# Kernel tuning notes

Measured on AMD Instinct MI355X. Metric: run time of the kernel, lower is better.

Reference implementation:

```python
import jax, jax.numpy as jnp
import numpy as np

DX, DZ, DT = 10.0, 10.0, 1.0e-3
NX, NZ = 512, 512
NSTEPS, NREC = 512, 128
DT2 = DT * DT
INV_DXDZ = 1.0 / (DX * DZ)


def setup_inputs() -> dict:
    key = jax.random.key(0)
    k1, k2, k3, k4 = jax.random.split(key, 4)
    # velocity in [1500, 2500] m/s -> CFL stable with dt=1e-3, dx=dz=10
    velocity_model = 1500.0 + 1000.0 * jax.random.uniform(k1, (NX, NZ), dtype=jnp.float32)
    source = jax.random.normal(k2, (NSTEPS,), dtype=jnp.float32)
    rec_x = jax.random.randint(k3, (NREC,), 0, NX)
    rec_z = jax.random.randint(k4, (NREC,), 0, NZ)
    return {
        "velocity_model": velocity_model,
        "source": source,
        "src_x": 256,
        "src_z": 8,
        "rec_x": rec_x,
        "rec_z": rec_z,
    }


def _laplacian(p):
    # 3x3 cross stencil with zero padding, scaled by 1/(dx*dz) -- identical to
    # F.conv2d(p, [[0,1,0],[1,-4,1],[0,1,0]]/(dx*dz), padding=1)
    pp = jnp.pad(p, 1)
    return (pp[:-2, 1:-1] + pp[2:, 1:-1] + pp[1:-1, :-2] + pp[1:-1, 2:] - 4.0 * p) * INV_DXDZ


def reference(velocity_model, source, src_x, src_z, rec_x, rec_z):
    v2_dt2 = velocity_model * velocity_model * DT2  # [nx, nz]

    def step(carry, s_t):
        p, p_old = carry
        p_new = 2.0 * p - p_old + v2_dt2 * _laplacian(p)
        p_new = p_new.at[src_x, src_z].add(s_t * DT2)
        return (p_new, p), p_new[rec_x, rec_z]  # gather all receivers at once

    p0 = jnp.zeros((NX, NZ), dtype=velocity_model.dtype)
    _, recs = jax.lax.scan(step, (p0, p0), source)  # recs: [n_steps, n_rec]
    return recs.T  # seismogram: [n_rec, n_steps]
```

## Files before the change

### kernel.cpp

```cpp
#include <hip/hip_runtime.h>


#define NXd 512
#define NZd 512
#define NSTEPSd 512
#define NRECd 128
#define DT2f 1.0e-6f
#define INVf 1.0e-2f
#define TBk 16
#define TIk 32
#define EXTk 64
#define NTILEk 16

__device__ __forceinline__ float dpp_shr1(float x) {
    int v = __builtin_amdgcn_update_dpp(0, __builtin_bit_cast(int, x),
                                        0x138, 0xF, 0xF, false);
    return __builtin_bit_cast(float, v);
}
__device__ __forceinline__ float dpp_shl1(float x) {
    int v = __builtin_amdgcn_update_dpp(0, __builtin_bit_cast(int, x),
                                        0x130, 0xF, 0xF, false);
    return __builtin_bit_cast(float, v);
}

__global__ __launch_bounds__(1024) void fdtd_tblock(
    const float* __restrict__ vel,
    const float* __restrict__ source,
    const int* __restrict__ src_x, const int* __restrict__ src_z,
    const int* __restrict__ rec_x, const int* __restrict__ rec_z,
    const float2* __restrict__ Pin, float2* __restrict__ Pout,
    float* __restrict__ out, int t0)
{
    __shared__ float sb[2][EXTk * EXTk];

    const int tid = threadIdx.x;
    const int w   = tid >> 6;
    const int ez  = tid & 63;
    const int gx0 = blockIdx.y * TIk, gz0 = blockIdx.x * TIk;
    const int ox = gx0 - TBk, oz = gz0 - TBk;
    const int gz = oz + ez;
    const bool zin = (gz >= 0 && gz < NZd);
    const int sx = *src_x, sz = *src_z;

    bool rOwn = false; int rIdx = 0;
    if (tid < NRECd) {
        int rx = rec_x[tid], rz = rec_z[tid];
        rOwn = (rx >= gx0 && rx < gx0 + TIk && rz >= gz0 && rz < gz0 + TIk);
        rIdx = (rx - ox) * EXTk + (rz - oz);
    }

    {
        int dxm = max(0, max(ox - sx, sx - (ox + EXTk - 1)));
        int dzm = max(0, max(oz - sz, sz - (oz + EXTk - 1)));
        if (dxm + dzm > t0 + TBk + 1) {
            if (rOwn) {
                #pragma unroll
                for (int s = 0; s < TBk; ++s)
                    out[tid * NSTEPSd + t0 + s] = 0.0f;
            }
            return;
        }
    }

    float rCur[4], rOld[4], rV2i[4];
    #pragma unroll
    for (int i = 0; i < 4; ++i) {
        const int ex = 4 * w + i;
        const int gx = ox + ex;
        float c = 0.0f, o = 0.0f, v2 = 0.0f;
        if (zin && gx >= 0 && gx < NXd) {
            const int g = gx * NZd + gz;
            float2 co = Pin[g];
            c = co.x; o = co.y;
            const float v = vel[g];
            v2 = v * v * (DT2f * INVf);
        }
        rCur[i] = c; rOld[i] = o; rV2i[i] = v2;
        sb[0][ex * EXTk + ez] = c;
    }
    const int rowUp = (w == 0)  ? 0        : 4 * w - 1;
    const int rowDn = (w == 15) ? EXTk - 1 : 4 * w + 4;

    const int exs = sx - ox, ezs = sz - oz;
    const bool srcHere = (exs >= 0 && exs < EXTk && ezs >= 0 && ezs < EXTk) &&
                         (tid == (((exs >> 2) << 6) | ezs));
    float sv[TBk];
    if (srcHere) {
        #pragma unroll
        for (int s = 0; s < TBk; ++s) sv[s] = source[t0 + s] * DT2f;
    }

    __syncthreads();

    float rv[TBk];
    #pragma unroll
    for (int s = 0; s < TBk; ++s) {
        const float* cur = sb[s & 1];
        float* nxt = sb[(s & 1) ^ 1];
        const float up0 = cur[rowUp * EXTk + ez];
        const float dn3 = cur[rowDn * EXTk + ez];
        float nv[4];
        #pragma unroll
        for (int i = 0; i < 4; ++i) {
            const float up = (i == 0) ? up0 : rCur[i - 1];
            const float dn = (i == 3) ? dn3 : rCur[i + 1];
            const float lf = dpp_shr1(rCur[i]);
            const float rt = dpp_shl1(rCur[i]);
            const float sum = (up + dn) + (lf + rt);
            const float t4 = __builtin_fmaf(-4.0f, rCur[i], sum);
            const float pm = __builtin_fmaf(2.0f, rCur[i], -rOld[i]);
            nv[i] = __builtin_fmaf(rV2i[i], t4, pm);
        }
        #pragma unroll
        for (int i = 0; i < 4; ++i) {
            rOld[i] = rCur[i];
            rCur[i] = nv[i];
            nxt[(4 * w + i) * EXTk + ez] = nv[i];
        }
        if (srcHere) {
            #pragma unroll
            for (int i = 0; i < 4; ++i) {
                if (i == (exs & 3)) {
                    rCur[i] += sv[s];
                    nxt[exs * EXTk + ezs] = rCur[i];
                }
            }
        }
        __syncthreads();
        if (rOwn) rv[s] = nxt[rIdx];
    }

    if (rOwn) {
        #pragma unroll
        for (int s = 0; s < TBk; ++s)
            out[tid * NSTEPSd + t0 + s] = rv[s];
    }

    if (w >= 4 && w < 12 && ez >= TBk && ez < EXTk - TBk) {
        #pragma unroll
        for (int i = 0; i < 4; ++i) {
            const int g = (ox + 4 * w + i) * NZd + gz;
            Pout[g] = make_float2(rCur[i], rOld[i]);
        }
    }
}

extern "C" void kernel_launch(void* const* d_in, const int* in_sizes, int n_in,
                              void* d_out, int out_size, void* d_ws, size_t ws_size,
                              hipStream_t stream) {
    const float* vel    = (const float*)d_in[0];
    const float* source = (const float*)d_in[1];
    const int*   src_x  = (const int*)d_in[2];
    const int*   src_z  = (const int*)d_in[3];
    const int*   rec_x  = (const int*)d_in[4];
    const int*   rec_z  = (const int*)d_in[5];
    float* out = (float*)d_out;

    const size_t F = (size_t)NXd * NZd;
    float2* PA = (float2*)d_ws;
    float2* PB = PA + F;

    hipMemsetAsync(d_ws, 0, 2 * F * sizeof(float2), stream);

    dim3 grid(NTILEk, NTILEk), block(1024);
    for (int k = 0; k < NSTEPSd / TBk; ++k) {
        const float2* Pin = (k & 1) ? PB : PA;
        float2* Pout      = (k & 1) ? PA : PB;
        fdtd_tblock<<<grid, block, 0, stream>>>(vel, source, src_x, src_z,
                                                rec_x, rec_z, Pin, Pout,
                                                out, k * TBk);
    }
}
```

Before: 365.0 us.

## Advance two time steps per barrier using redundant halo-row computation in registers

Each thread now reads two halo rows above and below from shared memory and also computes the neighbouring rows, so it can take two time steps per shared-memory exchange and cut the number of barriers and LDS round trips in half. Receivers are routed through shared-memory tables to the thread that owns the point, so readings come from registers instead of from LDS after each step. The cost is extra redundant arithmetic, more registers, extra global loads for the halo rows, and an atomic-based routing setup.

```diff
diff --git a/kernel.cpp b/kernel.cpp
--- a/kernel.cpp
+++ b/kernel.cpp
@@ -23,6 +23,20 @@
     return __builtin_bit_cast(float, v);
 }
 
+__device__ __forceinline__ float upd(float c, float o, float v2,
+                                     float up, float dn) {
+    float lf = dpp_shr1(c);
+    float rt = dpp_shl1(c);
+    float sum = (up + dn) + (lf + rt);
+    float t4 = __builtin_fmaf(-4.0f, c, sum);
+    float pm = __builtin_fmaf(2.0f, c, -o);
+    return __builtin_fmaf(v2, t4, pm);
+}
+
+__device__ __forceinline__ float sel4(int r, float a, float b, float c, float d) {
+    return (r == 0) ? a : (r == 1) ? b : (r == 2) ? c : d;
+}
+
 __global__ __launch_bounds__(1024) void fdtd_tblock(
     const float* __restrict__ vel,
     const float* __restrict__ source,
@@ -32,6 +46,7 @@
     float* __restrict__ out, int t0)
 {
     __shared__ float sb[2][EXTk * EXTk];
+    __shared__ int route0[1024], route1[1024], route2[1024];
 
     const int tid = threadIdx.x;
     const int w   = tid >> 6;
@@ -42,32 +57,27 @@
     const bool zin = (gz >= 0 && gz < NZd);
     const int sx = *src_x, sz = *src_z;
 
-    bool rOwn = false; int rIdx = 0;
-    if (tid < NRECd) {
-        int rx = rec_x[tid], rz = rec_z[tid];
-        rOwn = (rx >= gx0 && rx < gx0 + TIk && rz >= gz0 && rz < gz0 + TIk);
-        rIdx = (rx - ox) * EXTk + (rz - oz);
-    }
-
     {
         int dxm = max(0, max(ox - sx, sx - (ox + EXTk - 1)));
         int dzm = max(0, max(oz - sz, sz - (oz + EXTk - 1)));
         if (dxm + dzm > t0 + TBk + 1) {
-            if (rOwn) {
-                #pragma unroll
-                for (int s = 0; s < TBk; ++s)
-                    out[tid * NSTEPSd + t0 + s] = 0.0f;
+            if (tid < NRECd) {
+                int rx = rec_x[tid], rz = rec_z[tid];
+                if (rx >= gx0 && rx < gx0 + TIk && rz >= gz0 && rz < gz0 + TIk) {
+                    #pragma unroll
+                    for (int s = 0; s < TBk; ++s)
+                        out[tid * NSTEPSd + t0 + s] = 0.0f;
+                }
             }
             return;
         }
     }
 
-    float rCur[4], rOld[4], rV2i[4];
+    float rCur[4], rOld[4], rV2[4];
     #pragma unroll
     for (int i = 0; i < 4; ++i) {
-        const int ex = 4 * w + i;
-        const int gx = ox + ex;
-        float c = 0.0f, o = 0.0f, v2 = 0.0f;
+        const int gx = ox + 4 * w + i;
+        float c = 0.f, o = 0.f, v2 = 0.f;
         if (zin && gx >= 0 && gx < NXd) {
             const int g = gx * NZd + gz;
             float2 co = Pin[g];
@@ -75,65 +85,109 @@
             const float v = vel[g];
             v2 = v * v * (DT2f * INVf);
         }
-        rCur[i] = c; rOld[i] = o; rV2i[i] = v2;
-        sb[0][ex * EXTk + ez] = c;
-    }
-    const int rowUp = (w == 0)  ? 0        : 4 * w - 1;
-    const int rowDn = (w == 15) ? EXTk - 1 : 4 * w + 4;
+        rCur[i] = c; rOld[i] = o; rV2[i] = v2;
+        sb[0][(4 * w + i) * EXTk + ez] = c;
+    }
+    float rOldX0 = 0.f, rV2X0 = 0.f, rOldX1 = 0.f, rV2X1 = 0.f;
+    {
+        const int gxA = ox + 4 * w - 1;
+        if (w > 0 && zin && gxA >= 0 && gxA < NXd) {
+            const int g = gxA * NZd + gz;
+            rOldX0 = Pin[g].y;
+            float v = vel[g]; rV2X0 = v * v * (DT2f * INVf);
+        }
+        const int gxB = ox + 4 * w + 4;
+        if (w < 15 && zin && gxB >= 0 && gxB < NXd) {
+            const int g = gxB * NZd + gz;
+            rOldX1 = Pin[g].y;
+            float v = vel[g]; rV2X1 = v * v * (DT2f * INVf);
+        }
+    }
+
+    route0[tid] = -1; route1[tid] = -1; route2[tid] = -1;
+    __syncthreads();
+    if (tid < NRECd) {
+        int rx = rec_x[tid], rz = rec_z[tid];
+        if (rx >= gx0 && rx < gx0 + TIk && rz >= gz0 && rz < gz0 + TIk) {
+            int exr = rx - ox, exc = rz - oz;
+            int owner = ((exr >> 2) << 6) | exc;
+            int pack = (tid << 2) | (exr & 3);
+            int prev = atomicExch(&route0[owner], pack);
+            if (prev != -1) {
+                prev = atomicExch(&route1[owner], prev);
+                if (prev != -1) atomicExch(&route2[owner], prev);
+            }
+        }
+    }
+    __syncthreads();
+    const int myR0 = route0[tid], myR1 = route1[tid], myR2 = route2[tid];
 
     const int exs = sx - ox, ezs = sz - oz;
-    const bool srcHere = (exs >= 0 && exs < EXTk && ezs >= 0 && ezs < EXTk) &&
-                         (tid == (((exs >> 2) << 6) | ezs));
-    float sv[TBk];
-    if (srcHere) {
-        #pragma unroll
-        for (int s = 0; s < TBk; ++s) sv[s] = source[t0 + s] * DT2f;
-    }
-
-    __syncthreads();
+    const bool srcNear = (exs >= -1 && exs <= EXTk && ezs >= 0 && ezs < EXTk);
+
+    const int lb = 4 * w * EXTk + ez;
 
     float rv[TBk];
     #pragma unroll
-    for (int s = 0; s < TBk; ++s) {
-        const float* cur = sb[s & 1];
-        float* nxt = sb[(s & 1) ^ 1];
-        const float up0 = cur[rowUp * EXTk + ez];
-        const float dn3 = cur[rowDn * EXTk + ez];
-        float nv[4];
-        #pragma unroll
-        for (int i = 0; i < 4; ++i) {
-            const float up = (i == 0) ? up0 : rCur[i - 1];
-            const float dn = (i == 3) ? dn3 : rCur[i + 1];
-            const float lf = dpp_shr1(rCur[i]);
-            const float rt = dpp_shl1(rCur[i]);
-            const float sum = (up + dn) + (lf + rt);
-            const float t4 = __builtin_fmaf(-4.0f, rCur[i], sum);
-            const float pm = __builtin_fmaf(2.0f, rCur[i], -rOld[i]);
-            nv[i] = __builtin_fmaf(rV2i[i], t4, pm);
-        }
-        #pragma unroll
-        for (int i = 0; i < 4; ++i) {
-            rOld[i] = rCur[i];
-            rCur[i] = nv[i];
-            nxt[(4 * w + i) * EXTk + ez] = nv[i];
-        }
-        if (srcHere) {
-            #pragma unroll
-            for (int i = 0; i < 4; ++i) {
-                if (i == (exs & 3)) {
-                    rCur[i] += sv[s];
-                    nxt[exs * EXTk + ezs] = rCur[i];
-                }
-            }
-        }
+    for (int r = 0; r < TBk / 2; ++r) {
+        const float* cb = sb[r & 1];
+        float* nb = sb[(r & 1) ^ 1];
+        const float cUp2 = (w > 0)  ? cb[lb - 2 * EXTk] : 0.f;
+        const float cUp1 = (w > 0)  ? cb[lb - EXTk]     : 0.f;
+        const float cDn1 = (w < 15) ? cb[lb + 4 * EXTk] : 0.f;
+        const float cDn2 = (w < 15) ? cb[lb + 5 * EXTk] : 0.f;
+
+        float a0 = upd(cUp1,    rOldX0,  rV2X0,  cUp2,    rCur[0]);
+        float a1 = upd(rCur[0], rOld[0], rV2[0], cUp1,    rCur[1]);
+        float a2 = upd(rCur[1], rOld[1], rV2[1], rCur[0], rCur[2]);
+        float a3 = upd(rCur[2], rOld[2], rV2[2], rCur[1], rCur[3]);
+        float a4 = upd(rCur[3], rOld[3], rV2[3], rCur[2], cDn1);
+        float a5 = upd(cDn1,    rOldX1,  rV2X1,  rCur[3], cDn2);
+        if (srcNear && ez == ezs) {
+            const float svA = source[t0 + 2 * r] * DT2f;
+            const int d = exs - (4 * w - 1);
+            if (d == 0) a0 += svA; else if (d == 1) a1 += svA;
+            else if (d == 2) a2 += svA; else if (d == 3) a3 += svA;
+            else if (d == 4) a4 += svA; else if (d == 5) a5 += svA;
+        }
+        if (myR0 >= 0) rv[2 * r] = sel4(myR0 & 3, a1, a2, a3, a4);
+        if (myR1 >= 0) out[(myR1 >> 2) * NSTEPSd + t0 + 2 * r] =
+                            sel4(myR1 & 3, a1, a2, a3, a4);
+        if (myR2 >= 0) out[(myR2 >> 2) * NSTEPSd + t0 + 2 * r] =
+                            sel4(myR2 & 3, a1, a2, a3, a4);
+        rOldX0 = a0; rOldX1 = a5;
+
+        float b0 = upd(a1, rCur[0], rV2[0], a0, a2);
+        float b1 = upd(a2, rCur[1], rV2[1], a1, a3);
+        float b2 = upd(a3, rCur[2], rV2[2], a2, a4);
+        float b3 = upd(a4, rCur[3], rV2[3], a3, a5);
+        if (srcNear && ez == ezs && (exs >> 2) == w) {
+            const float svB = source[t0 + 2 * r + 1] * DT2f;
+            const int i = exs & 3;
+            if (i == 0) b0 += svB; else if (i == 1) b1 += svB;
+            else if (i == 2) b2 += svB; else b3 += svB;
+        }
+        rOld[0] = a1; rCur[0] = b0;
+        rOld[1] = a2; rCur[1] = b1;
+        rOld[2] = a3; rCur[2] = b2;
+        rOld[3] = a4; rCur[3] = b3;
+        if (myR0 >= 0) rv[2 * r + 1] = sel4(myR0 & 3, b0, b1, b2, b3);
+        if (myR1 >= 0) out[(myR1 >> 2) * NSTEPSd + t0 + 2 * r + 1] =
+                            sel4(myR1 & 3, b0, b1, b2, b3);
+        if (myR2 >= 0) out[(myR2 >> 2) * NSTEPSd + t0 + 2 * r + 1] =
+                            sel4(myR2 & 3, b0, b1, b2, b3);
+        nb[lb]            = b0;
+        nb[lb + EXTk]     = b1;
+        nb[lb + 2 * EXTk] = b2;
+        nb[lb + 3 * EXTk] = b3;
         __syncthreads();
-        if (rOwn) rv[s] = nxt[rIdx];
-    }
-
-    if (rOwn) {
+    }
+
+    if (myR0 >= 0) {
+        const int rec = myR0 >> 2;
         #pragma unroll
         for (int s = 0; s < TBk; ++s)
-            out[tid * NSTEPSd + t0 + s] = rv[s];
+            out[rec * NSTEPSd + t0 + s] = rv[s];
     }
 
     if (w >= 4 && w < 12 && ez >= TBk && ez < EXTk - TBk) {
```

Measured after the change: 442.3 us. 1.21x slower.

## Pack v2 coefficient into float4 field state and pad shared tile rows

Applied to the files above, without the earlier changes.

Adds an init kernel that precomputes v^2*dt^2/dxdz once and stores it with the current and previous pressure in a float4 per cell, replacing the separate float2 state plus per-launch velocity load and squaring. The shared-memory tile gains a zero row above and below, so halo reads use fixed offsets instead of clamped row indices. The global writeback is moved before the receiver output store. The tradeoff is more bytes per cell (16 vs 8 plus 4), with one vector load per cell instead of two loads.

```diff
diff --git a/kernel.cpp b/kernel.cpp
--- a/kernel.cpp
+++ b/kernel.cpp
@@ -11,6 +11,7 @@
 #define TIk 32
 #define EXTk 64
 #define NTILEk 16
+#define LROWS 66
 
 __device__ __forceinline__ float dpp_shr1(float x) {
     int v = __builtin_amdgcn_update_dpp(0, __builtin_bit_cast(int, x),
@@ -23,15 +24,26 @@
     return __builtin_bit_cast(float, v);
 }
 
+__global__ __launch_bounds__(256) void fdtd_init(const float* __restrict__ vel,
+                                                 float4* __restrict__ PA,
+                                                 float4* __restrict__ PB) {
+    int i = blockIdx.x * blockDim.x + threadIdx.x;
+    if (i < NXd * NZd) {
+        float v = vel[i];
+        float4 s = make_float4(0.f, 0.f, v * v * (DT2f * INVf), 0.f);
+        PA[i] = s;
+        PB[i] = s;
+    }
+}
+
 __global__ __launch_bounds__(1024) void fdtd_tblock(
-    const float* __restrict__ vel,
     const float* __restrict__ source,
     const int* __restrict__ src_x, const int* __restrict__ src_z,
     const int* __restrict__ rec_x, const int* __restrict__ rec_z,
-    const float2* __restrict__ Pin, float2* __restrict__ Pout,
+    const float4* __restrict__ Pin, float4* __restrict__ Pout,
     float* __restrict__ out, int t0)
 {
-    __shared__ float sb[2][EXTk * EXTk];
+    __shared__ float sb[2][LROWS * EXTk];
 
     const int tid = threadIdx.x;
     const int w   = tid >> 6;
@@ -46,7 +58,7 @@
     if (tid < NRECd) {
         int rx = rec_x[tid], rz = rec_z[tid];
         rOwn = (rx >= gx0 && rx < gx0 + TIk && rz >= gz0 && rz < gz0 + TIk);
-        rIdx = (rx - ox) * EXTk + (rz - oz);
+        rIdx = (rx - ox + 1) * EXTk + (rz - oz);
     }
 
     {
@@ -65,21 +77,21 @@
     float rCur[4], rOld[4], rV2i[4];
     #pragma unroll
     for (int i = 0; i < 4; ++i) {
-        const int ex = 4 * w + i;
-        const int gx = ox + ex;
-        float c = 0.0f, o = 0.0f, v2 = 0.0f;
+        const int gx = ox + 4 * w + i;
+        float c = 0.f, o = 0.f, v2 = 0.f;
         if (zin && gx >= 0 && gx < NXd) {
-            const int g = gx * NZd + gz;
-            float2 co = Pin[g];
-            c = co.x; o = co.y;
-            const float v = vel[g];
-            v2 = v * v * (DT2f * INVf);
+            float4 s = Pin[gx * NZd + gz];
+            c = s.x; o = s.y; v2 = s.z;
         }
         rCur[i] = c; rOld[i] = o; rV2i[i] = v2;
-        sb[0][ex * EXTk + ez] = c;
+        sb[0][(4 * w + 1 + i) * EXTk + ez] = c;
     }
-    const int rowUp = (w == 0)  ? 0        : 4 * w - 1;
-    const int rowDn = (w == 15) ? EXTk - 1 : 4 * w + 4;
+    if (w == 0) {
+        sb[0][ez] = 0.f;
+        sb[0][65 * EXTk + ez] = 0.f;
+        sb[1][ez] = 0.f;
+        sb[1][65 * EXTk + ez] = 0.f;
+    }
 
     const int exs = sx - ox, ezs = sz - oz;
     const bool srcHere = (exs >= 0 && exs < EXTk && ezs >= 0 && ezs < EXTk) &&
@@ -92,13 +104,15 @@
 
     __syncthreads();
 
+    const int fbase = 4 * w * EXTk + ez;
+
     float rv[TBk];
     #pragma unroll
     for (int s = 0; s < TBk; ++s) {
         const float* cur = sb[s & 1];
         float* nxt = sb[(s & 1) ^ 1];
-        const float up0 = cur[rowUp * EXTk + ez];
-        const float dn3 = cur[rowDn * EXTk + ez];
+        const float up0 = cur[fbase];
+        const float dn3 = cur[fbase + 5 * EXTk];
         float nv[4];
         #pragma unroll
         for (int i = 0; i < 4; ++i) {
@@ -115,14 +129,14 @@
         for (int i = 0; i < 4; ++i) {
             rOld[i] = rCur[i];
             rCur[i] = nv[i];
-            nxt[(4 * w + i) * EXTk + ez] = nv[i];
+            nxt[fbase + (1 + i) * EXTk] = nv[i];
         }
         if (srcHere) {
             #pragma unroll
             for (int i = 0; i < 4; ++i) {
                 if (i == (exs & 3)) {
                     rCur[i] += sv[s];
-                    nxt[exs * EXTk + ezs] = rCur[i];
+                    nxt[(exs + 1) * EXTk + ezs] = rCur[i];
                 }
             }
         }
@@ -130,18 +144,18 @@
         if (rOwn) rv[s] = nxt[rIdx];
     }
 
+    if (w >= 4 && w < 12 && ez >= TBk && ez < EXTk - TBk) {
+        #pragma unroll
+        for (int i = 0; i < 4; ++i) {
+            const int g = (ox + 4 * w + i) * NZd + gz;
+            Pout[g] = make_float4(rCur[i], rOld[i], rV2i[i], 0.f);
+        }
+    }
+
     if (rOwn) {
         #pragma unroll
         for (int s = 0; s < TBk; ++s)
             out[tid * NSTEPSd + t0 + s] = rv[s];
-    }
-
-    if (w >= 4 && w < 12 && ez >= TBk && ez < EXTk - TBk) {
-        #pragma unroll
-        for (int i = 0; i < 4; ++i) {
-            const int g = (ox + 4 * w + i) * NZd + gz;
-            Pout[g] = make_float2(rCur[i], rOld[i]);
-        }
     }
 }
 
@@ -157,16 +171,16 @@
     float* out = (float*)d_out;
 
     const size_t F = (size_t)NXd * NZd;
-    float2* PA = (float2*)d_ws;
-    float2* PB = PA + F;
+    float4* PA = (float4*)d_ws;
+    float4* PB = PA + F;
 
-    hipMemsetAsync(d_ws, 0, 2 * F * sizeof(float2), stream);
+    fdtd_init<<<(NXd * NZd + 255) / 256, 256, 0, stream>>>(vel, PA, PB);
 
     dim3 grid(NTILEk, NTILEk), block(1024);
     for (int k = 0; k < NSTEPSd / TBk; ++k) {
-        const float2* Pin = (k & 1) ? PB : PA;
-        float2* Pout      = (k & 1) ? PA : PB;
-        fdtd_tblock<<<grid, block, 0, stream>>>(vel, source, src_x, src_z,
+        const float4* Pin = (k & 1) ? PB : PA;
+        float4* Pout      = (k & 1) ? PA : PB;
+        fdtd_tblock<<<grid, block, 0, stream>>>(source, src_x, src_z,
                                                 rec_x, rec_z, Pin, Pout,
                                                 out, k * TBk);
     }
```

Result: slower. 384.7 us (+5.4%).

## Shrink x-tile to 16 rows with 512-thread blocks and padded LDS halo rows

Applied to the files above, without the earlier changes.

Changes the temporal-blocking tile from a 32x32 interior (64x64 extended) to 16x32 (48x64 extended), run by 512-thread blocks where each wave owns 6 rows instead of 4. Zero halo rows in LDS remove the boundary-row branches. The grid doubles to 512 blocks, which raises occupancy and parallelism across CUs. In exchange the redundant halo recompute per useful cell goes up, because the x-extent overhead ratio is now 48/16 instead of 64/32.

```diff
diff --git a/kernel.cpp b/kernel.cpp
--- a/kernel.cpp
+++ b/kernel.cpp
@@ -8,9 +8,13 @@
 #define DT2f 1.0e-6f
 #define INVf 1.0e-2f
 #define TBk 16
-#define TIk 32
-#define EXTk 64
-#define NTILEk 16
+#define TIXk 16
+#define TIZk 32
+#define EXTXk 48
+#define EXTZk 64
+#define NTXk 32
+#define NTZk 16
+#define LROWS 50
 
 __device__ __forceinline__ float dpp_shr1(float x) {
     int v = __builtin_amdgcn_update_dpp(0, __builtin_bit_cast(int, x),
@@ -23,7 +27,7 @@
     return __builtin_bit_cast(float, v);
 }
 
-__global__ __launch_bounds__(1024) void fdtd_tblock(
+__global__ __launch_bounds__(512) void fdtd_tblock(
     const float* __restrict__ vel,
     const float* __restrict__ source,
     const int* __restrict__ src_x, const int* __restrict__ src_z,
@@ -31,12 +35,12 @@
     const float2* __restrict__ Pin, float2* __restrict__ Pout,
     float* __restrict__ out, int t0)
 {
-    __shared__ float sb[2][EXTk * EXTk];
+    __shared__ float sb[2][LROWS * EXTZk];
 
     const int tid = threadIdx.x;
     const int w   = tid >> 6;
     const int ez  = tid & 63;
-    const int gx0 = blockIdx.y * TIk, gz0 = blockIdx.x * TIk;
+    const int gx0 = blockIdx.y * TIXk, gz0 = blockIdx.x * TIZk;
     const int ox = gx0 - TBk, oz = gz0 - TBk;
     const int gz = oz + ez;
     const bool zin = (gz >= 0 && gz < NZd);
@@ -45,13 +49,13 @@
     bool rOwn = false; int rIdx = 0;
     if (tid < NRECd) {
         int rx = rec_x[tid], rz = rec_z[tid];
-        rOwn = (rx >= gx0 && rx < gx0 + TIk && rz >= gz0 && rz < gz0 + TIk);
-        rIdx = (rx - ox) * EXTk + (rz - oz);
+        rOwn = (rx >= gx0 && rx < gx0 + TIXk && rz >= gz0 && rz < gz0 + TIZk);
+        rIdx = (rx - ox + 1) * EXTZk + (rz - oz);
     }
 
     {
-        int dxm = max(0, max(ox - sx, sx - (ox + EXTk - 1)));
-        int dzm = max(0, max(oz - sz, sz - (oz + EXTk - 1)));
+        int dxm = max(0, max(ox - sx, sx - (ox + EXTXk - 1)));
+        int dzm = max(0, max(oz - sz, sz - (oz + EXTZk - 1)));
         if (dxm + dzm > t0 + TBk + 1) {
             if (rOwn) {
                 #pragma unroll
@@ -62,12 +66,11 @@
         }
     }
 
-    float rCur[4], rOld[4], rV2i[4];
+    float rCur[6], rOld[6], rV2i[6];
     #pragma unroll
-    for (int i = 0; i < 4; ++i) {
-        const int ex = 4 * w + i;
-        const int gx = ox + ex;
-        float c = 0.0f, o = 0.0f, v2 = 0.0f;
+    for (int i = 0; i < 6; ++i) {
+        const int gx = ox + 6 * w + i;
+        float c = 0.f, o = 0.f, v2 = 0.f;
         if (zin && gx >= 0 && gx < NXd) {
             const int g = gx * NZd + gz;
             float2 co = Pin[g];
@@ -76,14 +79,20 @@
             v2 = v * v * (DT2f * INVf);
         }
         rCur[i] = c; rOld[i] = o; rV2i[i] = v2;
-        sb[0][ex * EXTk + ez] = c;
+        sb[0][(6 * w + 1 + i) * EXTZk + ez] = c;
     }
-    const int rowUp = (w == 0)  ? 0        : 4 * w - 1;
-    const int rowDn = (w == 15) ? EXTk - 1 : 4 * w + 4;
+    if (w == 0) {
+        sb[0][ez] = 0.f;
+        sb[0][(LROWS - 1) * EXTZk + ez] = 0.f;
+        sb[1][ez] = 0.f;
+        sb[1][(LROWS - 1) * EXTZk + ez] = 0.f;
+    }
 
     const int exs = sx - ox, ezs = sz - oz;
-    const bool srcHere = (exs >= 0 && exs < EXTk && ezs >= 0 && ezs < EXTk) &&
-                         (tid == (((exs >> 2) << 6) | ezs));
+    const int ws = exs >= 0 ? exs / 6 : 0;
+    const int srcI = exs - 6 * ws;
+    const bool srcHere = (exs >= 0 && exs < EXTXk && ezs >= 0 && ezs < EXTZk) &&
+                         (tid == ((ws << 6) | ezs));
     float sv[TBk];
     if (srcHere) {
         #pragma unroll
@@ -92,18 +101,20 @@
 
     __syncthreads();
 
+    const int fbase = 6 * w * EXTZk + ez;
+
     float rv[TBk];
     #pragma unroll
     for (int s = 0; s < TBk; ++s) {
         const float* cur = sb[s & 1];
         float* nxt = sb[(s & 1) ^ 1];
-        const float up0 = cur[rowUp * EXTk + ez];
-        const float dn3 = cur[rowDn * EXTk + ez];
-        float nv[4];
+        const float up0 = cur[fbase];
+        const float dn5 = cur[fbase + 7 * EXTZk];
+        float nv[6];
         #pragma unroll
-        for (int i = 0; i < 4; ++i) {
+        for (int i = 0; i < 6; ++i) {
             const float up = (i == 0) ? up0 : rCur[i - 1];
-            const float dn = (i == 3) ? dn3 : rCur[i + 1];
+            const float dn = (i == 5) ? dn5 : rCur[i + 1];
             const float lf = dpp_shr1(rCur[i]);
             const float rt = dpp_shl1(rCur[i]);
             const float sum = (up + dn) + (lf + rt);
@@ -112,17 +123,17 @@
             nv[i] = __builtin_fmaf(rV2i[i], t4, pm);
         }
         #pragma unroll
-        for (int i = 0; i < 4; ++i) {
+        for (int i = 0; i < 6; ++i) {
             rOld[i] = rCur[i];
             rCur[i] = nv[i];
-            nxt[(4 * w + i) * EXTk + ez] = nv[i];
+            nxt[fbase + (1 + i) * EXTZk] = nv[i];
         }
         if (srcHere) {
             #pragma unroll
-            for (int i = 0; i < 4; ++i) {
-                if (i == (exs & 3)) {
+            for (int i = 0; i < 6; ++i) {
+                if (i == srcI) {
                     rCur[i] += sv[s];
-                    nxt[exs * EXTk + ezs] = rCur[i];
+                    nxt[(exs + 1) * EXTZk + ezs] = rCur[i];
                 }
             }
         }
@@ -130,18 +141,21 @@
         if (rOwn) rv[s] = nxt[rIdx];
     }
 
+    if (ez >= TBk && ez < EXTZk - TBk) {
+        #pragma unroll
+        for (int i = 0; i < 6; ++i) {
+            const int fr = 6 * w + i;
+            if (fr >= TBk && fr < TBk + TIXk) {
+                const int g = (ox + fr) * NZd + gz;
+                Pout[g] = make_float2(rCur[i], rOld[i]);
+            }
+        }
+    }
+
     if (rOwn) {
         #pragma unroll
         for (int s = 0; s < TBk; ++s)
             out[tid * NSTEPSd + t0 + s] = rv[s];
-    }
-
-    if (w >= 4 && w < 12 && ez >= TBk && ez < EXTk - TBk) {
-        #pragma unroll
-        for (int i = 0; i < 4; ++i) {
-            const int g = (ox + 4 * w + i) * NZd + gz;
-            Pout[g] = make_float2(rCur[i], rOld[i]);
-        }
     }
 }
 
@@ -162,7 +176,7 @@
 
     hipMemsetAsync(d_ws, 0, 2 * F * sizeof(float2), stream);
 
-    dim3 grid(NTILEk, NTILEk), block(1024);
+    dim3 grid(NTZk, NTXk), block(512);
     for (int k = 0; k < NSTEPSd / TBk; ++k) {
         const float2* Pin = (k & 1) ? PB : PA;
         float2* Pout      = (k & 1) ? PA : PB;
```

Result: slower. 434.9 us (+19.2%).
